# Performance work log

Measured on AMD Instinct MI355X. Metric: run time of the kernel, lower is better.

## Reference

```python
import jax, jax.numpy as jnp
import numpy as np

N = 100000   # nodes
E = 1600000  # edges
IN = 128     # in_dim
H = 64       # hidden_dim
EPS = 1e-5


def layer_norm(x, g, b):
    mu = x.mean(-1, keepdims=True)
    v = ((x - mu) ** 2).mean(-1, keepdims=True)
    return (x - mu) * jax.lax.rsqrt(v + EPS) * g + b


def gcn_conv(x, W, b, src, dst, dinv):
    # PyG GCNConv: x' = D^{-1/2}(A+I)D^{-1/2} X W + b (degrees include self-loops)
    h = x @ W                                   # [N, H]
    coef = dinv[src] * dinv[dst]                # [E]
    agg = jax.ops.segment_sum(h[src] * coef[:, None], dst, num_segments=N)
    agg = agg + h * (dinv * dinv)[:, None]      # self-loop term
    return agg + b


def setup_inputs() -> dict:
    key = jax.random.key(0)
    ks = jax.random.split(key, 12)
    inp = {
        "x": jax.random.normal(ks[0], (N, IN), jnp.float32),
        "edge_index": jax.random.randint(ks[1], (2, E), 0, N, dtype=jnp.int64
                                         if jax.config.jax_enable_x64 else jnp.int32),
    }
    dims = [(IN, H), (H, H), (H, H)]
    for i, (di, do) in enumerate(dims, start=1):
        inp[f"W{i}"] = jax.random.normal(ks[2 * i], (di, do), jnp.float32) / np.sqrt(di)
        inp[f"b{i}"] = jnp.zeros((do,), jnp.float32)
        inp[f"g{i}"] = jnp.ones((do,), jnp.float32)
        inp[f"be{i}"] = jnp.zeros((do,), jnp.float32)
    inp["Wh"] = jax.random.normal(ks[11], (H, 1), jnp.float32) / np.sqrt(H)
    inp["bh"] = jnp.zeros((1,), jnp.float32)
    return inp


def reference(x, edge_index, W1, b1, g1, be1, W2, b2, g2, be2, W3, b3, g3, be3, Wh, bh):
    src, dst = edge_index[0], edge_index[1]
    deg = jax.ops.segment_sum(jnp.ones((E,), x.dtype), dst, num_segments=N) + 1.0
    dinv = jax.lax.rsqrt(deg)
    for W, b, g, be in ((W1, b1, g1, be1), (W2, b2, g2, be2), (W3, b3, g3, be3)):
        x = gcn_conv(x, W, b, src, dst, dinv)
        x = layer_norm(x, g, be)
        x = jax.nn.gelu(x, approximate=False)  # F.gelu default = exact erf
        # dropout omitted (eval mode / deterministic reference)
    return (x @ Wh + bh).squeeze(-1)  # [N]
```

## Files before the change

### kernel.cpp

```cpp
#include <hip/hip_runtime.h>
#include <math.h>

#define NODES 100000
#define EDGES 1600000
#define NBUCK 196
#define BCAP2 12288
#define EPB 4096
#define BINB 391
#define GEMMB 1563

typedef __attribute__((ext_vector_type(8))) short short8;
typedef __attribute__((ext_vector_type(4))) float floatx4;
typedef __attribute__((ext_vector_type(4))) unsigned uv4;

__device__ __forceinline__ float gsum8(float x) {
#pragma unroll
  for (int o = 4; o > 0; o >>= 1) x += __shfl_xor(x, o, 64);
  return x;
}

__device__ __forceinline__ short f2bf(float f) {
  union { float f; unsigned u; } v;
  v.f = f;
  unsigned r = 0x7fffu + ((v.u >> 16) & 1u);
  return (short)((v.u + r) >> 16);
}
__device__ __forceinline__ float bflo(unsigned p) {
  union { unsigned u; float f; } v; v.u = p << 16; return v.f;
}
__device__ __forceinline__ float bfhi(unsigned p) {
  union { unsigned u; float f; } v; v.u = p & 0xffff0000u; return v.f;
}
__device__ __forceinline__ unsigned scale2(unsigned p, float s) {
  float lo = bflo(p) * s, hi = bfhi(p) * s;
  unsigned ulo = (unsigned)(unsigned short)f2bf(lo);
  unsigned uhi = (unsigned)(unsigned short)f2bf(hi);
  return ulo | (uhi << 16);
}

#define BIN_SMEM (4 * 256 * 4 + EPB * 4 + EPB)
__device__ __forceinline__ void bin_body(char* smemraw, int b, const int* __restrict__ src,
                                         const int* __restrict__ dst, int* __restrict__ bins,
                                         int* __restrict__ gcur) {
  int* cnt = (int*)smemraw;
  int* gb = cnt + 256;
  int* lb = gb + 256;
  int* lcur = lb + 256;
  int* rec = lcur + 256;
  unsigned char* rbk = (unsigned char*)(rec + EPB);
  int t = threadIdx.x;
  cnt[t] = 0;
  __syncthreads();
  int base = b * EPB;
  int nv = EDGES - base; if (nv > EPB) nv = EPB;
  int s[16], d[16];
#pragma unroll
  for (int j = 0; j < 16; ++j) {
    int e = base + j * 256 + t;
    if (e < EDGES) {
      s[j] = src[e];
      d[j] = dst[e];
      atomicAdd(&cnt[d[j] >> 9], 1);
    } else {
      d[j] = -1;
    }
  }
  __syncthreads();
  int c = cnt[t];
  lb[t] = c;
  __syncthreads();
  for (int o = 1; o < 256; o <<= 1) {
    int u = (t >= o) ? lb[t - o] : 0;
    __syncthreads();
    lb[t] += u;
    __syncthreads();
  }
  int ex = lb[t] - c;
  gb[t] = (c > 0) ? atomicAdd(&gcur[t], c) : 0;
  __syncthreads();
  lb[t] = ex;
  lcur[t] = ex;
  __syncthreads();
#pragma unroll
  for (int j = 0; j < 16; ++j) {
    if (d[j] >= 0) {
      int bk = d[j] >> 9;
      int lp = atomicAdd(&lcur[bk], 1);
      rec[lp] = s[j] | ((d[j] & 511) << 17);
      rbk[lp] = (unsigned char)bk;
    }
  }
  __syncthreads();
  for (int i = t; i < nv; i += 256) {
    int bk = rbk[i];
    int pos = gb[bk] + (i - lb[bk]);
    if (pos < BCAP2) bins[bk * BCAP2 + pos] = rec[i];
  }
}

#define FILL_SMEM (256 * 4 + 512 * 4 + 512 * 4 + 4 * 4 + BCAP2 * 4 + 512 * 4)
__device__ __forceinline__ void fill_body(char* smemraw, int b, const int* __restrict__ bins,
                                          const int* __restrict__ gcur, int* __restrict__ rowptr,
                                          float* __restrict__ dinv, int* __restrict__ csr,
                                          short* __restrict__ hs) {
  int* bsm = (int*)smemraw;
  int* cnt = bsm + 256;
  int* cur = cnt + 512;
  int* wtot = cur + 512;
  int* stage = wtot + 4;
  float* dinvs = (float*)(stage + BCAP2);
  int t = threadIdx.x;
  int v = 0;
  if (t < NBUCK) { v = gcur[t]; if (v > BCAP2) v = BCAP2; }
  bsm[t] = v;
  cnt[t] = 0; cnt[t + 256] = 0;
  __syncthreads();
  for (int o = 1; o < 256; o <<= 1) {
    int u = (t >= o) ? bsm[t - o] : 0;
    __syncthreads();
    bsm[t] += u;
    __syncthreads();
  }
  if (b == 0 && t == NBUCK - 1) rowptr[NODES] = bsm[t];
  int cb = gcur[b]; if (cb > BCAP2) cb = BCAP2;
  int bbase = bsm[b] - cb;
  const int* bp = &bins[(size_t)b * BCAP2];
  for (int i = t; i < cb; i += 256)
    atomicAdd(&cnt[(bp[i] >> 17) & 511], 1);
  __syncthreads();
  int a0 = cnt[2 * t], a1 = cnt[2 * t + 1];
  int sum2 = a0 + a1;
  int lane = t & 63, w = t >> 6;
  int inc = sum2;
#pragma unroll
  for (int o = 1; o < 64; o <<= 1) {
    int u = __shfl_up(inc, o, 64);
    if (lane >= o) inc += u;
  }
  if (lane == 63) wtot[w] = inc;
  __syncthreads();
  int wpre = 0;
  for (int ww = 0; ww < w; ++ww) wpre += wtot[ww];
  int l0 = wpre + inc - sum2;
  int l1 = l0 + a0;
  int n0 = b * 512 + 2 * t, n1 = n0 + 1;
  float dv0 = rsqrtf((float)a0 + 1.0f), dv1 = rsqrtf((float)a1 + 1.0f);
  if (n0 < NODES) { rowptr[n0] = bbase + l0; dinv[n0] = dv0; }
  if (n1 < NODES) { rowptr[n1] = bbase + l1; dinv[n1] = dv1; }
  dinvs[2 * t] = dv0; dinvs[2 * t + 1] = dv1;
  cur[2 * t] = l0; cur[2 * t + 1] = l1;
  __syncthreads();
  for (int i = t; i < cb; i += 256) {
    int pk = bp[i];
    int lp = atomicAdd(&cur[(pk >> 17) & 511], 1);
    stage[lp] = pk & 0x1FFFF;
  }
  __syncthreads();
  for (int i = t; i < cb; i += 256) csr[bbase + i] = stage[i];
  uv4* hv = (uv4*)hs;
  int nb = b * 512;
  for (int i = t; i < 4096; i += 256) {
    int row = i >> 3, ch = i & 7;
    int n = nb + row;
    if (n < NODES) {
      float s = dinvs[row];
      uv4 x = hv[(size_t)n * 8 + ch];
#pragma unroll
      for (int ww = 0; ww < 4; ++ww) x[ww] = scale2(x[ww], s);
      hv[(size_t)n * 8 + ch] = x;
    }
  }
}

#define GEMM_SMEM (64 * 136 * 2)
__device__ __forceinline__ void gemm_body(char* smemraw, int tile0, const float* __restrict__ x,
                                          const float* __restrict__ W, short* __restrict__ hs) {
  constexpr int K = 128, KP = K + 8;
  short* wt = (short*)smemraw;
  for (int idx = threadIdx.x; idx < K * 64; idx += 256) {
    int k = idx >> 6, n = idx & 63;
    wt[n * KP + k] = f2bf(W[idx]);
  }
  __syncthreads();
  int wid = threadIdx.x >> 6, lane = threadIdx.x & 63;
  int tile = tile0 + wid;
  if (tile * 16 >= NODES) return;
  int m = lane & 15, q = lane >> 4;

  short8 bfr[4][K / 32];
#pragma unroll
  for (int ct = 0; ct < 4; ++ct)
#pragma unroll
    for (int ks = 0; ks < K / 32; ++ks)
      bfr[ct][ks] = *reinterpret_cast<const short8*>(&wt[(ct * 16 + m) * KP + ks * 32 + q * 8]);

  floatx4 acc[4];
#pragma unroll
  for (int ct = 0; ct < 4; ++ct) acc[ct] = {0.f, 0.f, 0.f, 0.f};
  int r0 = tile * 16;
#pragma unroll
  for (int ks = 0; ks < K / 32; ++ks) {
    const float* xp = &x[(size_t)(r0 + m) * K + ks * 32 + q * 8];
    floatx4 a0 = *reinterpret_cast<const floatx4*>(xp);
    floatx4 a1 = *reinterpret_cast<const floatx4*>(xp + 4);
    short8 af;
#pragma unroll
    for (int j = 0; j < 4; ++j) { af[j] = f2bf(a0[j]); af[4 + j] = f2bf(a1[j]); }
#pragma unroll
    for (int ct = 0; ct < 4; ++ct)
      acc[ct] = __builtin_amdgcn_mfma_f32_16x16x32_bf16(af, bfr[ct][ks], acc[ct], 0, 0, 0);
  }
#pragma unroll
  for (int ct = 0; ct < 4; ++ct)
#pragma unroll
    for (int r = 0; r < 4; ++r) {
      int row = r0 + q * 4 + r, col = ct * 16 + m;
      hs[row * 64 + col] = f2bf(acc[ct][r]);
    }
}

__device__ __forceinline__ void prepw_body(int p, const float* __restrict__ W2,
                                           const float* __restrict__ W3,
                                           short* __restrict__ wt2, short* __restrict__ wt3) {
  const float* W = (p < 4) ? W2 : W3;
  short* wt = (p < 4) ? wt2 : wt3;
  int b0 = (p & 3) * 1024;
  for (int i = threadIdx.x; i < 1024; i += 256) {
    int e = b0 + i;
    int k = e >> 6, n = e & 63;
    wt[n * 72 + k] = f2bf(W[e]);
  }
}

__device__ __forceinline__ void do_agg24(const uv4* __restrict__ hsv, const int* __restrict__ csr,
                                         int n, int e0, int e1, int lane, float acc[8]) {
  int q = lane & 7, srcb = lane & 0x38;
  uv4 sv = hsv[(size_t)n * 8 + q];
#pragma unroll
  for (int w = 0; w < 4; ++w) { acc[2 * w] = bflo(sv[w]); acc[2 * w + 1] = bfhi(sv[w]); }
  for (int base = e0; base < e1; base += 24) {
    int rem = e1 - base;
    int cnt = rem > 24 ? 24 : rem;
    int p0 = base + q, p1 = p0 + 8, p2 = p0 + 16;
    int i0 = csr[p0 < e1 ? p0 : e0];
    int i1 = csr[p1 < e1 ? p1 : e0];
    int i2 = csr[p2 < e1 ? p2 : e0];
    uv4 v[24];
#pragma unroll
    for (int j = 0; j < 8; ++j) {
      int s = __shfl(i0, srcb | j, 64);
      v[j] = hsv[(size_t)s * 8 + q];
    }
#pragma unroll
    for (int j = 0; j < 8; ++j) {
      int s = __shfl(i1, srcb | j, 64);
      v[8 + j] = hsv[(size_t)s * 8 + q];
    }
#pragma unroll
    for (int j = 0; j < 8; ++j) {
      int s = __shfl(i2, srcb | j, 64);
      v[16 + j] = hsv[(size_t)s * 8 + q];
    }
    __builtin_amdgcn_sched_barrier(0);
    if (cnt == 24) {
#pragma unroll
      for (int j = 0; j < 24; ++j)
#pragma unroll
        for (int w = 0; w < 4; ++w) { acc[2 * w] += bflo(v[j][w]); acc[2 * w + 1] += bfhi(v[j][w]); }
    } else {
#pragma unroll
      for (int j = 0; j < 24; ++j)
        if (j < cnt)
#pragma unroll
          for (int w = 0; w < 4; ++w) { acc[2 * w] += bflo(v[j][w]); acc[2 * w + 1] += bfhi(v[j][w]); }
    }
  }
}

__global__ __launch_bounds__(256, 1) void k_aggg(const short* __restrict__ hs,
                                                 const float* __restrict__ dinv,
                                                 const int* __restrict__ rowptr,
                                                 const int* __restrict__ csr,
                                                 const float* __restrict__ bias,
                                                 const float* __restrict__ gam,
                                                 const float* __restrict__ bet,
                                                 const short* __restrict__ wtg,
                                                 short* __restrict__ hsn) {
  __shared__ __align__(16) short wt[64 * 72];
  __shared__ __align__(16) short ut[32 * 72];
  int t = threadIdx.x;
  {
    const int* wp = (const int*)wtg;
    int* wd = (int*)wt;
    for (int idx = t; idx < 2304; idx += 256) wd[idx] = wp[idx];
  }
  const uv4* hsv = (const uv4*)hs;
  int lane = t & 63, wid = t >> 6;
  int g = lane >> 3, q = lane & 7;
  int nb0 = blockIdx.x * 32;
  int r = wid * 8 + g;
  int n = nb0 + r;
  int e0 = rowptr[n], e1 = rowptr[n + 1];
  float dn = dinv[n];
  float acc[8];
  do_agg24(hsv, csr, n, e0, e1, lane, acc);

  const floatx4* bi4 = (const floatx4*)bias;
  floatx4 b0 = bi4[q * 2], b1 = bi4[q * 2 + 1];
#pragma unroll
  for (int f = 0; f < 4; ++f) { acc[f] = acc[f] * dn + b0[f]; acc[f + 4] = acc[f + 4] * dn + b1[f]; }

  float lsum = 0.f;
#pragma unroll
  for (int f = 0; f < 8; ++f) lsum += acc[f];
  float mu = gsum8(lsum) * (1.0f / 64.0f);
  float d[8], lvar = 0.f;
#pragma unroll
  for (int f = 0; f < 8; ++f) { d[f] = acc[f] - mu; lvar += d[f] * d[f]; }
  float rs = rsqrtf(gsum8(lvar) * (1.0f / 64.0f) + 1e-5f);
  const floatx4* gm4 = (const floatx4*)gam;
  const floatx4* bt4 = (const floatx4*)bet;
  floatx4 g0 = gm4[q * 2], g1 = gm4[q * 2 + 1];
  floatx4 t0 = bt4[q * 2], t1 = bt4[q * 2 + 1];
  short8 us;
#pragma unroll
  for (int f = 0; f < 8; ++f) {
    float gv = (f < 4) ? g0[f] : g1[f - 4];
    float tv = (f < 4) ? t0[f] : t1[f - 4];
    float vv = d[f] * rs * gv + tv;
    float u = 0.5f * vv * (1.0f + erff(vv * 0.70710678118654752f));
    us[f] = f2bf(u * dn);
  }
  *reinterpret_cast<short8*>(&ut[r * 72 + q * 8]) = us;
  __syncthreads();

  int m = lane & 15, q2 = lane >> 4;
  int tile = wid >> 1, cb = (wid & 1) * 2;
  short8 bfr[2][2];
#pragma unroll
  for (int ct = 0; ct < 2; ++ct)
#pragma unroll
    for (int ks = 0; ks < 2; ++ks)
      bfr[ct][ks] = *reinterpret_cast<const short8*>(&wt[((cb + ct) * 16 + m) * 72 + ks * 32 + q2 * 8]);
  floatx4 ac[2];
#pragma unroll
  for (int ct = 0; ct < 2; ++ct) ac[ct] = {0.f, 0.f, 0.f, 0.f};
#pragma unroll
  for (int ks = 0; ks < 2; ++ks) {
    short8 af = *reinterpret_cast<const short8*>(&ut[(tile * 16 + m) * 72 + ks * 32 + q2 * 8]);
#pragma unroll
    for (int ct = 0; ct < 2; ++ct)
      ac[ct] = __builtin_amdgcn_mfma_f32_16x16x32_bf16(af, bfr[ct][ks], ac[ct], 0, 0, 0);
  }
#pragma unroll
  for (int ct = 0; ct < 2; ++ct)
#pragma unroll
    for (int rr = 0; rr < 4; ++rr) {
      int row = nb0 + tile * 16 + q2 * 4 + rr, col = (cb + ct) * 16 + m;
      hsn[row * 64 + col] = f2bf(ac[ct][rr]);
    }
}

__global__ __launch_bounds__(256, 1) void k_agg_fin(const short* __restrict__ hs,
                                                    const float* __restrict__ dinv,
                                                    const int* __restrict__ rowptr,
                                                    const int* __restrict__ csr,
                                                    const float* __restrict__ bias,
                                                    const float* __restrict__ gam,
                                                    const float* __restrict__ bet,
                                                    const float* __restrict__ Wh,
                                                    const float* __restrict__ bh,
                                                    float* __restrict__ out) {
  const uv4* hsv = (const uv4*)hs;
  int lane = threadIdx.x & 63, wid = threadIdx.x >> 6;
  int g = lane >> 3, q = lane & 7;
  int n = blockIdx.x * 32 + wid * 8 + g;
  int e0 = rowptr[n], e1 = rowptr[n + 1];
  float dn = dinv[n];
  float acc[8];
  do_agg24(hsv, csr, n, e0, e1, lane, acc);
  const floatx4* bi4 = (const floatx4*)bias;
  floatx4 b0 = bi4[q * 2], b1 = bi4[q * 2 + 1];
#pragma unroll
  for (int f = 0; f < 4; ++f) { acc[f] = acc[f] * dn + b0[f]; acc[f + 4] = acc[f + 4] * dn + b1[f]; }
  float lsum = 0.f;
#pragma unroll
  for (int f = 0; f < 8; ++f) lsum += acc[f];
  float mu = gsum8(lsum) * (1.0f / 64.0f);
  float d[8], lvar = 0.f;
#pragma unroll
  for (int f = 0; f < 8; ++f) { d[f] = acc[f] - mu; lvar += d[f] * d[f]; }
  float rs = rsqrtf(gsum8(lvar) * (1.0f / 64.0f) + 1e-5f);
  const floatx4* gm4 = (const floatx4*)gam;
  const floatx4* bt4 = (const floatx4*)bet;
  floatx4 g0 = gm4[q * 2], g1 = gm4[q * 2 + 1];
  floatx4 t0 = bt4[q * 2], t1 = bt4[q * 2 + 1];
  const floatx4* wh4 = (const floatx4*)Wh;
  floatx4 w0 = wh4[q * 2], w1 = wh4[q * 2 + 1];
  float lp = 0.f;
#pragma unroll
  for (int f = 0; f < 8; ++f) {
    float gv = (f < 4) ? g0[f] : g1[f - 4];
    float tv = (f < 4) ? t0[f] : t1[f - 4];
    float wv = (f < 4) ? w0[f] : w1[f - 4];
    float vv = d[f] * rs * gv + tv;
    float u = 0.5f * vv * (1.0f + erff(vv * 0.70710678118654752f));
    lp += u * wv;
  }
  float p = gsum8(lp);
  if (q == 0) out[n] = p + bh[0];
}

__global__ __launch_bounds__(256) void k_pre1(const int* __restrict__ src, const int* __restrict__ dst,
                                              int* __restrict__ bins, int* __restrict__ gcur,
                                              const float* __restrict__ x, const float* __restrict__ W1,
                                              short* __restrict__ hs,
                                              const float* __restrict__ W2, const float* __restrict__ W3,
                                              short* __restrict__ wt2, short* __restrict__ wt3) {
  __shared__ __align__(16) char smem[BIN_SMEM];
  int b = blockIdx.x;
  if (b < BINB) bin_body(smem, b, src, dst, bins, gcur);
  else if (b < BINB + GEMMB) gemm_body(smem, (b - BINB) * 4, x, W1, hs);
  else prepw_body(b - BINB - GEMMB, W2, W3, wt2, wt3);
}

__global__ __launch_bounds__(256) void k_pre2(const int* __restrict__ bins, const int* __restrict__ gcur,
                                              int* __restrict__ rowptr, float* __restrict__ dinv,
                                              int* __restrict__ csr, short* __restrict__ hs) {
  __shared__ __align__(16) char smem[FILL_SMEM];
  fill_body(smem, blockIdx.x, bins, gcur, rowptr, dinv, csr, hs);
}

__global__ __launch_bounds__(256) void k_bin2(const int* src, const int* dst, int* bins, int* gcur) {
  __shared__ __align__(16) char smem[BIN_SMEM];
  bin_body(smem, blockIdx.x, src, dst, bins, gcur);
}
__global__ __launch_bounds__(256) void k_fillb2(const int* bins, const int* gcur, int* rowptr,
                                                float* dinv, int* csr, short* hs) {
  __shared__ __align__(16) char smem[FILL_SMEM];
  fill_body(smem, blockIdx.x, bins, gcur, rowptr, dinv, csr, hs);
}
__global__ __launch_bounds__(256) void k_gemm(const float* x, const float* W, short* hs) {
  __shared__ __align__(16) char smem[GEMM_SMEM];
  gemm_body(smem, blockIdx.x * 4, x, W, hs);
}
__global__ __launch_bounds__(256) void k_prepw(const float* W2, const float* W3, short* wt2, short* wt3) {
  prepw_body(blockIdx.x, W2, W3, wt2, wt3);
}

extern "C" void kernel_launch(void* const* d_in, const int* in_sizes, int n_in,
                              void* d_out, int out_size, void* d_ws, size_t ws_size,
                              hipStream_t stream) {
  const float* x  = (const float*)d_in[0];
  const int* ei   = (const int*)d_in[1];
  const float* W1 = (const float*)d_in[2];
  const float* b1 = (const float*)d_in[3];
  const float* g1 = (const float*)d_in[4];
  const float* be1= (const float*)d_in[5];
  const float* W2 = (const float*)d_in[6];
  const float* b2 = (const float*)d_in[7];
  const float* g2 = (const float*)d_in[8];
  const float* be2= (const float*)d_in[9];
  const float* W3 = (const float*)d_in[10];
  const float* b3 = (const float*)d_in[11];
  const float* g3 = (const float*)d_in[12];
  const float* be3= (const float*)d_in[13];
  const float* Wh = (const float*)d_in[14];
  const float* bh = (const float*)d_in[15];
  const int* srcp = ei;
  const int* dstp = ei + EDGES;

  char* ws = (char*)d_ws;
  size_t off = 0;
  auto take = [&](size_t bytes) {
    char* p = ws + off;
    off = (off + bytes + 255) & ~(size_t)255;
    return p;
  };
  float* dinv = (float*)take((size_t)NODES * 4);
  int* rowptr = (int*)take((size_t)(NODES + 1) * 4);
  int* csr    = (int*)take((size_t)EDGES * 4);
  short* hs_a = (short*)take((size_t)NODES * 64 * 2);
  short* hs_b = (short*)take((size_t)NODES * 64 * 2);
  short* wt2  = (short*)take((size_t)64 * 72 * 2);
  short* wt3  = (short*)take((size_t)64 * 72 * 2);

  size_t bins_sz = (size_t)NBUCK * BCAP2 * 4;
  bool overlap = (ws_size >= off + bins_sz + 4096);
  int* bins; int* gcur;
  if (overlap) {
    bins = (int*)take(bins_sz);
    gcur = (int*)take((size_t)NBUCK * 4);
  } else {
    bins = (int*)hs_a;
    gcur = (int*)hs_b;
  }

  (void)hipMemsetAsync(gcur, 0, (size_t)NBUCK * 4, stream);
  if (overlap) {
    k_pre1<<<BINB + GEMMB + 8, 256, 0, stream>>>(srcp, dstp, bins, gcur, x, W1, hs_a, W2, W3, wt2, wt3);
    k_pre2<<<NBUCK, 256, 0, stream>>>(bins, gcur, rowptr, dinv, csr, hs_a);
  } else {
    k_bin2<<<BINB, 256, 0, stream>>>(srcp, dstp, bins, gcur);
    k_gemm<<<GEMMB, 256, 0, stream>>>(x, W1, hs_a);
    k_prepw<<<8, 256, 0, stream>>>(W2, W3, wt2, wt3);
    k_fillb2<<<NBUCK, 256, 0, stream>>>(bins, gcur, rowptr, dinv, csr, hs_a);
  }
  k_aggg<<<NODES / 32, 256, 0, stream>>>(hs_a, dinv, rowptr, csr, b1, g1, be1, wt2, hs_b);
  k_aggg<<<NODES / 32, 256, 0, stream>>>(hs_b, dinv, rowptr, csr, b2, g2, be2, wt3, hs_a);
  k_agg_fin<<<NODES / 32, 256, 0, stream>>>(hs_a, dinv, rowptr, csr, b3, g3, be3, Wh, bh, (float*)d_out);
}
```

Baseline: 281.5 us.

## Rework CSR build scans, pad bucket counters, shrink gather batch, relax launch bounds

Replaces the LDS Hillis-Steele scans in the binning and fill stages with wavefront shuffle scans. Pads the global bucket counters to a 16-int stride to avoid atomic contention on shared cache lines. Runs the fill kernel with 512 threads. Shrinks the aggregation gather from 24-edge to 8-edge batches and drops the min-blocks-per-CU launch bound so more waves can be resident. The aim is lower preprocessing sync overhead and higher occupancy in the aggregation kernels, at the cost of less memory-level parallelism per wave in the gather.

New measurement: 274.2 us. 1.03x faster.

```diff
diff --git a/kernel.cpp b/kernel.cpp
--- a/kernel.cpp
+++ b/kernel.cpp
@@ -8,6 +8,7 @@
 #define EPB 4096
 #define BINB 391
 #define GEMMB 1563
+#define GSTRIDE 16
 
 typedef __attribute__((ext_vector_type(8))) short short8;
 typedef __attribute__((ext_vector_type(4))) float floatx4;
@@ -38,7 +39,7 @@
   return ulo | (uhi << 16);
 }
 
-#define BIN_SMEM (4 * 256 * 4 + EPB * 4 + EPB)
+#define BIN_SMEM ((4 * 256 + 8) * 4 + EPB * 4 + EPB)
 __device__ __forceinline__ void bin_body(char* smemraw, int b, const int* __restrict__ src,
                                          const int* __restrict__ dst, int* __restrict__ bins,
                                          int* __restrict__ gcur) {
@@ -46,7 +47,8 @@
   int* gb = cnt + 256;
   int* lb = gb + 256;
   int* lcur = lb + 256;
-  int* rec = lcur + 256;
+  int* wt4 = lcur + 256;
+  int* rec = wt4 + 8;
   unsigned char* rbk = (unsigned char*)(rec + EPB);
   int t = threadIdx.x;
   cnt[t] = 0;
@@ -67,17 +69,19 @@
   }
   __syncthreads();
   int c = cnt[t];
-  lb[t] = c;
-  __syncthreads();
-  for (int o = 1; o < 256; o <<= 1) {
-    int u = (t >= o) ? lb[t - o] : 0;
-    __syncthreads();
-    lb[t] += u;
-    __syncthreads();
-  }
-  int ex = lb[t] - c;
-  gb[t] = (c > 0) ? atomicAdd(&gcur[t], c) : 0;
-  __syncthreads();
+  int lane = t & 63, w = t >> 6;
+  int inc = c;
+#pragma unroll
+  for (int o = 1; o < 64; o <<= 1) {
+    int u = __shfl_up(inc, o, 64);
+    if (lane >= o) inc += u;
+  }
+  if (lane == 63) wt4[w] = inc;
+  __syncthreads();
+  int wpre = 0;
+  for (int ww = 0; ww < w; ++ww) wpre += wt4[ww];
+  int ex = wpre + inc - c;
+  gb[t] = (c > 0) ? atomicAdd(&gcur[t * GSTRIDE], c) : 0;
   lb[t] = ex;
   lcur[t] = ex;
   __syncthreads();
@@ -98,7 +102,8 @@
   }
 }
 
-#define FILL_SMEM (256 * 4 + 512 * 4 + 512 * 4 + 4 * 4 + BCAP2 * 4 + 512 * 4)
+#define FILL_T 512
+#define FILL_SMEM ((256 + 512 + 512 + 8 + BCAP2 + 512) * 4)
 __device__ __forceinline__ void fill_body(char* smemraw, int b, const int* __restrict__ bins,
                                           const int* __restrict__ gcur, int* __restrict__ rowptr,
                                           float* __restrict__ dinv, int* __restrict__ csr,
@@ -107,59 +112,84 @@
   int* cnt = bsm + 256;
   int* cur = cnt + 512;
   int* wtot = cur + 512;
-  int* stage = wtot + 4;
+  int* stage = wtot + 8;
   float* dinvs = (float*)(stage + BCAP2);
   int t = threadIdx.x;
-  int v = 0;
-  if (t < NBUCK) { v = gcur[t]; if (v > BCAP2) v = BCAP2; }
-  bsm[t] = v;
-  cnt[t] = 0; cnt[t + 256] = 0;
-  __syncthreads();
-  for (int o = 1; o < 256; o <<= 1) {
-    int u = (t >= o) ? bsm[t - o] : 0;
-    __syncthreads();
-    bsm[t] += u;
-    __syncthreads();
-  }
+  int lane = t & 63, w = t >> 6;
+  if (t < 256) {
+    int v = 0;
+    if (t < NBUCK) { v = gcur[t * GSTRIDE]; if (v > BCAP2) v = BCAP2; }
+    int inc = v;
+#pragma unroll
+    for (int o = 1; o < 64; o <<= 1) {
+      int u = __shfl_up(inc, o, 64);
+      if (lane >= o) inc += u;
+    }
+    if (lane == 63) wtot[w] = inc;
+    cnt[t] = 0; cnt[t + 256] = 0;
+    bsm[t] = v;
+  }
+  __syncthreads();
+  if (t < 256) {
+    int wpre = 0;
+    for (int ww = 0; ww < w; ++ww) wpre += wtot[ww];
+    int v = bsm[t];
+    int inc = v;
+#pragma unroll
+    for (int o = 1; o < 64; o <<= 1) {
+      int u = __shfl_up(inc, o, 64);
+      if (lane >= o) inc += u;
+    }
+    bsm[t] = wpre + inc;
+  }
+  __syncthreads();
   if (b == 0 && t == NBUCK - 1) rowptr[NODES] = bsm[t];
-  int cb = gcur[b]; if (cb > BCAP2) cb = BCAP2;
+  int cb = gcur[b * GSTRIDE]; if (cb > BCAP2) cb = BCAP2;
   int bbase = bsm[b] - cb;
   const int* bp = &bins[(size_t)b * BCAP2];
-  for (int i = t; i < cb; i += 256)
+  for (int i = t; i < cb; i += FILL_T)
     atomicAdd(&cnt[(bp[i] >> 17) & 511], 1);
   __syncthreads();
-  int a0 = cnt[2 * t], a1 = cnt[2 * t + 1];
-  int sum2 = a0 + a1;
-  int lane = t & 63, w = t >> 6;
-  int inc = sum2;
-#pragma unroll
-  for (int o = 1; o < 64; o <<= 1) {
-    int u = __shfl_up(inc, o, 64);
-    if (lane >= o) inc += u;
-  }
-  if (lane == 63) wtot[w] = inc;
-  __syncthreads();
-  int wpre = 0;
-  for (int ww = 0; ww < w; ++ww) wpre += wtot[ww];
-  int l0 = wpre + inc - sum2;
-  int l1 = l0 + a0;
-  int n0 = b * 512 + 2 * t, n1 = n0 + 1;
-  float dv0 = rsqrtf((float)a0 + 1.0f), dv1 = rsqrtf((float)a1 + 1.0f);
-  if (n0 < NODES) { rowptr[n0] = bbase + l0; dinv[n0] = dv0; }
-  if (n1 < NODES) { rowptr[n1] = bbase + l1; dinv[n1] = dv1; }
-  dinvs[2 * t] = dv0; dinvs[2 * t + 1] = dv1;
-  cur[2 * t] = l0; cur[2 * t + 1] = l1;
-  __syncthreads();
-  for (int i = t; i < cb; i += 256) {
+  if (t < 256) {
+    int a0 = cnt[2 * t], a1 = cnt[2 * t + 1];
+    int sum2 = a0 + a1;
+    int inc = sum2;
+#pragma unroll
+    for (int o = 1; o < 64; o <<= 1) {
+      int u = __shfl_up(inc, o, 64);
+      if (lane >= o) inc += u;
+    }
+    if (lane == 63) wtot[w] = inc;
+    cur[2 * t] = inc - sum2;
+    cur[2 * t + 1] = a0;
+    dinvs[2 * t] = __int_as_float(a0);
+    dinvs[2 * t + 1] = __int_as_float(a1);
+  }
+  __syncthreads();
+  if (t < 256) {
+    int wpre = 0;
+    for (int ww = 0; ww < w; ++ww) wpre += wtot[ww];
+    int a0 = __float_as_int(dinvs[2 * t]), a1 = __float_as_int(dinvs[2 * t + 1]);
+    int l0 = wpre + cur[2 * t];
+    int l1 = l0 + a0;
+    int n0 = b * 512 + 2 * t, n1 = n0 + 1;
+    float dv0 = rsqrtf((float)a0 + 1.0f), dv1 = rsqrtf((float)a1 + 1.0f);
+    if (n0 < NODES) { rowptr[n0] = bbase + l0; dinv[n0] = dv0; }
+    if (n1 < NODES) { rowptr[n1] = bbase + l1; dinv[n1] = dv1; }
+    dinvs[2 * t] = dv0; dinvs[2 * t + 1] = dv1;
+    cur[2 * t] = l0; cur[2 * t + 1] = l1;
+  }
+  __syncthreads();
+  for (int i = t; i < cb; i += FILL_T) {
     int pk = bp[i];
     int lp = atomicAdd(&cur[(pk >> 17) & 511], 1);
     stage[lp] = pk & 0x1FFFF;
   }
   __syncthreads();
-  for (int i = t; i < cb; i += 256) csr[bbase + i] = stage[i];
+  for (int i = t; i < cb; i += FILL_T) csr[bbase + i] = stage[i];
   uv4* hv = (uv4*)hs;
   int nb = b * 512;
-  for (int i = t; i < 4096; i += 256) {
+  for (int i = t; i < 4096; i += FILL_T) {
     int row = i >> 3, ch = i & 7;
     int n = nb + row;
     if (n < NODES) {
@@ -232,44 +262,31 @@
   }
 }
 
-__device__ __forceinline__ void do_agg24(const uv4* __restrict__ hsv, const int* __restrict__ csr,
-                                         int n, int e0, int e1, int lane, float acc[8]) {
+__device__ __forceinline__ void do_agg(const uv4* __restrict__ hsv, const int* __restrict__ csr,
+                                       int n, int e0, int e1, int lane, float acc[8]) {
   int q = lane & 7, srcb = lane & 0x38;
   uv4 sv = hsv[(size_t)n * 8 + q];
 #pragma unroll
   for (int w = 0; w < 4; ++w) { acc[2 * w] = bflo(sv[w]); acc[2 * w + 1] = bfhi(sv[w]); }
-  for (int base = e0; base < e1; base += 24) {
-    int rem = e1 - base;
-    int cnt = rem > 24 ? 24 : rem;
-    int p0 = base + q, p1 = p0 + 8, p2 = p0 + 16;
-    int i0 = csr[p0 < e1 ? p0 : e0];
-    int i1 = csr[p1 < e1 ? p1 : e0];
-    int i2 = csr[p2 < e1 ? p2 : e0];
-    uv4 v[24];
-#pragma unroll
-    for (int j = 0; j < 8; ++j) {
-      int s = __shfl(i0, srcb | j, 64);
-      v[j] = hsv[(size_t)s * 8 + q];
-    }
-#pragma unroll
-    for (int j = 0; j < 8; ++j) {
-      int s = __shfl(i1, srcb | j, 64);
-      v[8 + j] = hsv[(size_t)s * 8 + q];
-    }
-#pragma unroll
-    for (int j = 0; j < 8; ++j) {
-      int s = __shfl(i2, srcb | j, 64);
-      v[16 + j] = hsv[(size_t)s * 8 + q];
-    }
-    __builtin_amdgcn_sched_barrier(0);
-    if (cnt == 24) {
-#pragma unroll
-      for (int j = 0; j < 24; ++j)
+  for (int base = e0; base < e1; base += 8) {
+    int cnt = e1 - base;
+    if (cnt > 8) cnt = 8;
+    int a = base + (q < cnt ? q : 0);
+    int sidx = csr[a];
+    int s[8];
+#pragma unroll
+    for (int j = 0; j < 8; ++j) s[j] = __shfl(sidx, srcb | j, 64);
+    uv4 v[8];
+#pragma unroll
+    for (int j = 0; j < 8; ++j) v[j] = hsv[(size_t)s[j] * 8 + q];
+    if (cnt == 8) {
+#pragma unroll
+      for (int j = 0; j < 8; ++j)
 #pragma unroll
         for (int w = 0; w < 4; ++w) { acc[2 * w] += bflo(v[j][w]); acc[2 * w + 1] += bfhi(v[j][w]); }
     } else {
 #pragma unroll
-      for (int j = 0; j < 24; ++j)
+      for (int j = 0; j < 8; ++j)
         if (j < cnt)
 #pragma unroll
           for (int w = 0; w < 4; ++w) { acc[2 * w] += bflo(v[j][w]); acc[2 * w + 1] += bfhi(v[j][w]); }
@@ -277,15 +294,15 @@
   }
 }
 
-__global__ __launch_bounds__(256, 1) void k_aggg(const short* __restrict__ hs,
-                                                 const float* __restrict__ dinv,
-                                                 const int* __restrict__ rowptr,
-                                                 const int* __restrict__ csr,
-                                                 const float* __restrict__ bias,
-                                                 const float* __restrict__ gam,
-                                                 const float* __restrict__ bet,
-                                                 const short* __restrict__ wtg,
-                                                 short* __restrict__ hsn) {
+__global__ __launch_bounds__(256) void k_aggg(const short* __restrict__ hs,
+                                              const float* __restrict__ dinv,
+                                              const int* __restrict__ rowptr,
+                                              const int* __restrict__ csr,
+                                              const float* __restrict__ bias,
+                                              const float* __restrict__ gam,
+                                              const float* __restrict__ bet,
+                                              const short* __restrict__ wtg,
+                                              short* __restrict__ hsn) {
   __shared__ __align__(16) short wt[64 * 72];
   __shared__ __align__(16) short ut[32 * 72];
   int t = threadIdx.x;
@@ -303,7 +320,7 @@
   int e0 = rowptr[n], e1 = rowptr[n + 1];
   float dn = dinv[n];
   float acc[8];
-  do_agg24(hsv, csr, n, e0, e1, lane, acc);
+  do_agg(hsv, csr, n, e0, e1, lane, acc);
 
   const floatx4* bi4 = (const floatx4*)bias;
   floatx4 b0 = bi4[q * 2], b1 = bi4[q * 2 + 1];
@@ -361,16 +378,16 @@
     }
 }
 
-__global__ __launch_bounds__(256, 1) void k_agg_fin(const short* __restrict__ hs,
-                                                    const float* __restrict__ dinv,
-                                                    const int* __restrict__ rowptr,
-                                                    const int* __restrict__ csr,
-                                                    const float* __restrict__ bias,
-                                                    const float* __restrict__ gam,
-                                                    const float* __restrict__ bet,
-                                                    const float* __restrict__ Wh,
-                                                    const float* __restrict__ bh,
-                                                    float* __restrict__ out) {
+__global__ __launch_bounds__(256) void k_agg_fin(const short* __restrict__ hs,
+                                                 const float* __restrict__ dinv,
+                                                 const int* __restrict__ rowptr,
+                                                 const int* __restrict__ csr,
+                                                 const float* __restrict__ bias,
+                                                 const float* __restrict__ gam,
+                                                 const float* __restrict__ bet,
+                                                 const float* __restrict__ Wh,
+                                                 const float* __restrict__ bh,
+                                                 float* __restrict__ out) {
   const uv4* hsv = (const uv4*)hs;
   int lane = threadIdx.x & 63, wid = threadIdx.x >> 6;
   int g = lane >> 3, q = lane & 7;
@@ -378,7 +395,7 @@
   int e0 = rowptr[n], e1 = rowptr[n + 1];
   float dn = dinv[n];
   float acc[8];
-  do_agg24(hsv, csr, n, e0, e1, lane, acc);
+  do_agg(hsv, csr, n, e0, e1, lane, acc);
   const floatx4* bi4 = (const floatx4*)bias;
   floatx4 b0 = bi4[q * 2], b1 = bi4[q * 2 + 1];
 #pragma unroll
@@ -424,9 +441,9 @@
   else prepw_body(b - BINB - GEMMB, W2, W3, wt2, wt3);
 }
 
-__global__ __launch_bounds__(256) void k_pre2(const int* __restrict__ bins, const int* __restrict__ gcur,
-                                              int* __restrict__ rowptr, float* __restrict__ dinv,
-                                              int* __restrict__ csr, short* __restrict__ hs) {
+__global__ __launch_bounds__(FILL_T) void k_pre2(const int* __restrict__ bins, const int* __restrict__ gcur,
+                                                 int* __restrict__ rowptr, float* __restrict__ dinv,
+                                                 int* __restrict__ csr, short* __restrict__ hs) {
   __shared__ __align__(16) char smem[FILL_SMEM];
   fill_body(smem, blockIdx.x, bins, gcur, rowptr, dinv, csr, hs);
 }
@@ -435,8 +452,8 @@
   __shared__ __align__(16) char smem[BIN_SMEM];
   bin_body(smem, blockIdx.x, src, dst, bins, gcur);
 }
-__global__ __launch_bounds__(256) void k_fillb2(const int* bins, const int* gcur, int* rowptr,
-                                                float* dinv, int* csr, short* hs) {
+__global__ __launch_bounds__(FILL_T) void k_fillb2(const int* bins, const int* gcur, int* rowptr,
+                                                   float* dinv, int* csr, short* hs) {
   __shared__ __align__(16) char smem[FILL_SMEM];
   fill_body(smem, blockIdx.x, bins, gcur, rowptr, dinv, csr, hs);
 }
@@ -486,25 +503,26 @@
   short* wt3  = (short*)take((size_t)64 * 72 * 2);
 
   size_t bins_sz = (size_t)NBUCK * BCAP2 * 4;
-  bool overlap = (ws_size >= off + bins_sz + 4096);
+  size_t gcur_sz = (size_t)NBUCK * GSTRIDE * 4;
+  bool overlap = (ws_size >= off + bins_sz + gcur_sz + 4096);
   int* bins; int* gcur;
   if (overlap) {
     bins = (int*)take(bins_sz);
-    gcur = (int*)take((size_t)NBUCK * 4);
+    gcur = (int*)take(gcur_sz);
   } else {
     bins = (int*)hs_a;
     gcur = (int*)hs_b;
   }
 
-  (void)hipMemsetAsync(gcur, 0, (size_t)NBUCK * 4, stream);
+  (void)hipMemsetAsync(gcur, 0, gcur_sz, stream);
   if (overlap) {
     k_pre1<<<BINB + GEMMB + 8, 256, 0, stream>>>(srcp, dstp, bins, gcur, x, W1, hs_a, W2, W3, wt2, wt3);
-    k_pre2<<<NBUCK, 256, 0, stream>>>(bins, gcur, rowptr, dinv, csr, hs_a);
+    k_pre2<<<NBUCK, FILL_T, 0, stream>>>(bins, gcur, rowptr, dinv, csr, hs_a);
   } else {
     k_bin2<<<BINB, 256, 0, stream>>>(srcp, dstp, bins, gcur);
     k_gemm<<<GEMMB, 256, 0, stream>>>(x, W1, hs_a);
     k_prepw<<<8, 256, 0, stream>>>(W2, W3, wt2, wt3);
-    k_fillb2<<<NBUCK, 256, 0, stream>>>(bins, gcur, rowptr, dinv, csr, hs_a);
+    k_fillb2<<<NBUCK, FILL_T, 0, stream>>>(bins, gcur, rowptr, dinv, csr, hs_a);
   }
   k_aggg<<<NODES / 32, 256, 0, stream>>>(hs_a, dinv, rowptr, csr, b1, g1, be1, wt2, hs_b);
   k_aggg<<<NODES / 32, 256, 0, stream>>>(hs_b, dinv, rowptr, csr, b2, g2, be2, wt3, hs_a);
```
